# Kernel tuning notes

Measured on AMD Instinct MI355X. Metric: run time of the kernel, lower is better.

## Reference

```python
import jax, jax.numpy as jnp
import numpy as np

# HashGrid config (from ExplicitMaterial.Config defaults)
N_LEVELS = 16
F_PER_LEVEL = 2
TABLE_SIZE = 1 << 19          # log2_hashmap_size = 19
BASE_RES = 16
GROWTH = 1.447269237440378
N_NEURONS = 64                # VanillaMLP hidden width
N_OUT = 3                     # n_output_dims
N_POINTS = 1048576

# 8 trilinear corner offsets, [8,3]
OFFSETS = np.stack(np.meshgrid([0, 1], [0, 1], [0, 1], indexing='ij'), -1).reshape(8, 3)
PRIMES = np.array([1, 2654435761, 805459861], dtype=np.uint32)  # tcnn spatial hash primes


def _level_params():
    # tcnn convention: scale = base * growth^l - 1, resolution = ceil(scale) + 1
    out = []
    for l in range(N_LEVELS):
        scale = BASE_RES * (GROWTH ** l) - 1.0
        res = int(np.ceil(scale)) + 1
        out.append((scale, res))
    return out


def hash_grid_encode(x01, table):
    # x01: [N,3] in [0,1]; table: [L, T, F]
    offsets_u = jnp.asarray(OFFSETS, dtype=jnp.uint32)          # [8,3]
    offsets_f = jnp.asarray(OFFSETS, dtype=x01.dtype)           # [8,3]
    outs = []
    for l, (scale, res) in enumerate(_level_params()):
        pos = x01 * scale + 0.5                                  # [N,3]
        p0f = jnp.floor(pos)
        frac = pos - p0f                                         # [N,3]
        p0 = p0f.astype(jnp.uint32)
        corners = p0[:, None, :] + offsets_u                     # [N,8,3]
        if res ** 3 <= TABLE_SIZE:
            # dense indexing for coarse levels
            c = jnp.minimum(corners, np.uint32(res - 1))
            idx = c[..., 0] + c[..., 1] * np.uint32(res) + c[..., 2] * np.uint32(res * res)
        else:
            # spatial hash: xor of coordinate * prime, masked to table size
            idx = (corners[..., 0] * np.uint32(PRIMES[0])) \
                ^ (corners[..., 1] * np.uint32(PRIMES[1])) \
                ^ (corners[..., 2] * np.uint32(PRIMES[2]))
            idx = idx & np.uint32(TABLE_SIZE - 1)
        feats = table[l][idx]                                    # [N,8,F] gather
        w = jnp.prod(jnp.where(offsets_f[None] > 0, frac[:, None, :], 1.0 - frac[:, None, :]), axis=-1)  # [N,8]
        outs.append(jnp.sum(w[..., None] * feats, axis=1))       # [N,F]
    return jnp.concatenate(outs, axis=-1)                        # [N, L*F]


def setup_inputs() -> dict:
    key = jax.random.key(0)
    k1, k2, k3, k4 = jax.random.split(key, 4)
    positions = jax.random.uniform(k1, (N_POINTS, 3), dtype=jnp.float32, minval=-1.0, maxval=1.0)
    # tcnn init: uniform(-1e-4, 1e-4)
    hash_table = jax.random.uniform(k2, (N_LEVELS, TABLE_SIZE, F_PER_LEVEL), dtype=jnp.float32,
                                    minval=-1e-4, maxval=1e-4)
    d_in = N_LEVELS * F_PER_LEVEL
    w1 = jax.random.normal(k3, (d_in, N_NEURONS), dtype=jnp.float32) * (2.0 / d_in) ** 0.5
    w2 = jax.random.normal(k4, (N_NEURONS, N_OUT), dtype=jnp.float32) * (2.0 / N_NEURONS) ** 0.5
    return {"positions": positions, "hash_table": hash_table, "w1": w1, "w2": w2}


def reference(positions, hash_table, w1, w2):
    # contract_to_unisphere (bounded): scale bbox [-1,1]^3 -> [0,1]^3
    x01 = (positions + 1.0) * 0.5
    enc = hash_grid_encode(x01, hash_table)                      # [N,32]
    h = jax.nn.relu(enc @ w1)                                    # VanillaMLP, bias-free
    feat = h @ w2                                                # output_activation = none
    color = jax.nn.sigmoid(feat)                                 # material_activation
    return color
```

## Files before the change

### kernel.cpp

```cpp
#include <hip/hip_runtime.h>
#include <stdint.h>
#include <math.h>

#define NLEVELS 16
#define NDENSE  5
#define NHASH   11
#define TSIZE   (1u << 19)
#define HMASK   (TSIZE - 1u)
#define PRIME_Y 2654435761u
#define PRIME_Z 805459861u

#define FP8_SCALE 8192.0f
#define FP8_INV   (1.0f / 8192.0f)

typedef float v2f __attribute__((ext_vector_type(2)));

struct Params {
    float    scale[NLEVELS];
    unsigned res[NDENSE];
    unsigned doff[NDENSE];
};

__device__ __forceinline__ unsigned umin_(unsigned a, unsigned b) { return a < b ? a : b; }

__global__ __launch_bounds__(256) void repack_hash8(const float4* __restrict__ src,
                                                    uint2* __restrict__ dst, int n4) {
    const int i = blockIdx.x * 256 + threadIdx.x;
    if (i >= n4) return;
    const float4 a = src[2 * i];
    const float4 b = src[2 * i + 1];
    int lo = __builtin_amdgcn_cvt_pk_fp8_f32(a.x * FP8_SCALE, a.y * FP8_SCALE, 0, false);
    lo     = __builtin_amdgcn_cvt_pk_fp8_f32(a.z * FP8_SCALE, a.w * FP8_SCALE, lo, true);
    int hi = __builtin_amdgcn_cvt_pk_fp8_f32(b.x * FP8_SCALE, b.y * FP8_SCALE, 0, false);
    hi     = __builtin_amdgcn_cvt_pk_fp8_f32(b.z * FP8_SCALE, b.w * FP8_SCALE, hi, true);
    dst[i] = make_uint2((unsigned)lo, (unsigned)hi);
}

__global__ __launch_bounds__(256) void repack_dense8(const float2* __restrict__ table,
                                                     uint2* __restrict__ dst, Params pr) {
    const int l = blockIdx.y;
    const unsigned R = pr.res[l];
    const unsigned n = R * R * R;
    const unsigned e = blockIdx.x * 256 + threadIdx.x;
    if (e >= n) return;
    const unsigned xx = e % R;
    const unsigned t  = e / R;
    const unsigned yy = t % R;
    const unsigned x1 = umin_(xx + 1u, R - 1) - xx;
    const unsigned y1 = (umin_(yy + 1u, R - 1) - yy) * R;
    const float2* src = table + (size_t)l * TSIZE;
    const float2 a = src[e];
    const float2 b = src[e + x1];
    const float2 c = src[e + y1];
    const float2 d = src[e + y1 + x1];
    int w0 = __builtin_amdgcn_cvt_pk_fp8_f32(a.x * FP8_SCALE, a.y * FP8_SCALE, 0, false);
    w0     = __builtin_amdgcn_cvt_pk_fp8_f32(b.x * FP8_SCALE, b.y * FP8_SCALE, w0, true);
    int w1 = __builtin_amdgcn_cvt_pk_fp8_f32(c.x * FP8_SCALE, c.y * FP8_SCALE, 0, false);
    w1     = __builtin_amdgcn_cvt_pk_fp8_f32(d.x * FP8_SCALE, d.y * FP8_SCALE, w1, true);
    dst[pr.doff[l] + e] = make_uint2((unsigned)w0, (unsigned)w1);
}

__device__ __forceinline__ void lvl_tw(float x, float y, float z, float s,
                                       float* wx, float* wy, float* wz) {
    const float fx = fmaf(x, s, 0.5f), fy = fmaf(y, s, 0.5f), fz = fmaf(z, s, 0.5f);
    const float tx = fx - floorf(fx), ty = fy - floorf(fy), tz = fz - floorf(fz);
    wx[0] = 1.f - tx; wx[1] = tx;
    wy[0] = 1.f - ty; wy[1] = ty;
    wz[0] = 1.f - tz; wz[1] = tz;
}

__device__ __forceinline__ void hash_issue_pair(const void* __restrict__ hashTV, int lrel,
                                                float x, float y, float z, float s,
                                                unsigned* __restrict__ U,
                                                unsigned* __restrict__ V,
                                                unsigned* __restrict__ flg) {
    const float fx = fmaf(x, s, 0.5f), fy = fmaf(y, s, 0.5f), fz = fmaf(z, s, 0.5f);
    const unsigned x0 = (unsigned)floorf(fx);
    const unsigned y0 = (unsigned)floorf(fy);
    const unsigned z0 = (unsigned)floorf(fz);
    const unsigned hy0 = y0 * PRIME_Y, hz0 = z0 * PRIME_Z;
    unsigned H[4];
    H[0] = hy0 ^ hz0;
    H[1] = (hy0 + PRIME_Y) ^ hz0;
    H[2] = hy0 ^ (hz0 + PRIME_Z);
    H[3] = (hy0 + PRIME_Y) ^ (hz0 + PRIME_Z);
    *flg = (x0 & 1u) | (((y0 ^ z0) & 1u) << 1);
    if (x0 & 1u) {
        const unsigned short* t8 = (const unsigned short*)hashTV + (size_t)lrel * TSIZE;
#pragma unroll
        for (int c = 0; c < 4; ++c) {
            const unsigned i0 = (x0 ^ H[c]) & HMASK;
            const unsigned i1 = ((x0 + 1u) ^ H[c]) & HMASK;
            U[c] = t8[i0];
            V[c] = t8[i1];
        }
    } else {
        const unsigned* t32 = (const unsigned*)hashTV + (size_t)lrel * (TSIZE / 2);
#pragma unroll
        for (int c = 0; c < 4; ++c) {
            const unsigned i0 = (x0 ^ H[c]) & HMASK;
            U[c] = t32[i0 >> 1];
        }
    }
}

__global__ __launch_bounds__(256) void hgmlp_fp8p(
    const float* __restrict__ gpos,
    const void* __restrict__ hashTV,
    const uint2* __restrict__ denseT,
    const float* __restrict__ gw1,
    const float* __restrict__ gw2,
    float* __restrict__ gout,
    int npts, Params pr)
{
    __shared__ float w1t[64 * 32];
    __shared__ float w2s[64 * 3];
    const int tid = threadIdx.x;
    const int p = blockIdx.x * 256 + tid;

    float px = 0.f, py = 0.f, pz = 0.f;
    if (p < npts) { px = gpos[3 * p]; py = gpos[3 * p + 1]; pz = gpos[3 * p + 2]; }

    for (int e = tid; e < 32 * 64; e += 256) {
        const int i = e & 31, j = e >> 5;
        w1t[e] = gw1[i * 64 + j];
    }
    if (tid < 192) w2s[tid] = gw2[tid];
    __syncthreads();

    if (p >= npts) return;

    const float x = (px + 1.f) * 0.5f;
    const float y = (py + 1.f) * 0.5f;
    const float z = (pz + 1.f) * 0.5f;

    float enc[32];

    uint2 dv[NDENSE][2];
#pragma unroll
    for (int l = 0; l < NDENSE; ++l) {
        const float s = pr.scale[l];
        const unsigned R = pr.res[l];
        const float fx = fmaf(x, s, 0.5f), fy = fmaf(y, s, 0.5f), fz = fmaf(z, s, 0.5f);
        const unsigned x0 = (unsigned)floorf(fx);
        const unsigned y0 = (unsigned)floorf(fy);
        const unsigned z0 = (unsigned)floorf(fz);
        const unsigned base = umin_(x0, R - 1) + umin_(y0, R - 1) * R;
        const unsigned cz0 = umin_(z0, R - 1) * R * R;
        const unsigned cz1 = umin_(z0 + 1u, R - 1) * R * R;
        const uint2* tl = denseT + pr.doff[l];
        dv[l][0] = tl[base + cz0];
        dv[l][1] = tl[base + cz1];
    }

    unsigned U[4][4], V[4][4], flg[4];
    hash_issue_pair(hashTV, 0, x, y, z, pr.scale[5], U[0], V[0], &flg[0]);
    hash_issue_pair(hashTV, 1, x, y, z, pr.scale[6], U[1], V[1], &flg[1]);
    hash_issue_pair(hashTV, 2, x, y, z, pr.scale[7], U[2], V[2], &flg[2]);

#pragma unroll
    for (int l = 0; l < NDENSE; ++l) {
        float wx[2], wy[2], wz[2];
        lvl_tw(x, y, z, pr.scale[l], wx, wy, wz);
        float e0 = 0.f, e1 = 0.f;
#pragma unroll
        for (int dz = 0; dz < 2; ++dz) {
            const uint2 u2 = dv[l][dz];
            const v2f c00 = __builtin_amdgcn_cvt_pk_f32_fp8((int)u2.x, false);
            const v2f c10 = __builtin_amdgcn_cvt_pk_f32_fp8((int)u2.x, true);
            const v2f c01 = __builtin_amdgcn_cvt_pk_f32_fp8((int)u2.y, false);
            const v2f c11 = __builtin_amdgcn_cvt_pk_f32_fp8((int)u2.y, true);
            const float w00 = wz[dz] * wy[0] * wx[0];
            const float w10 = wz[dz] * wy[0] * wx[1];
            const float w01 = wz[dz] * wy[1] * wx[0];
            const float w11 = wz[dz] * wy[1] * wx[1];
            e0 = fmaf(w00, c00.x, fmaf(w10, c10.x, fmaf(w01, c01.x, fmaf(w11, c11.x, e0))));
            e1 = fmaf(w00, c00.y, fmaf(w10, c10.y, fmaf(w01, c01.y, fmaf(w11, c11.y, e1))));
        }
        enc[2 * l + 0] = e0 * FP8_INV;
        enc[2 * l + 1] = e1 * FP8_INV;
    }

#pragma unroll
    for (int l = NDENSE; l < NLEVELS; ++l) {
        if (l + 3 < NLEVELS) {
            const int sl = (l + 3 - NDENSE) & 3;
            hash_issue_pair(hashTV, l + 3 - NDENSE, x, y, z, pr.scale[l + 3],
                            U[sl], V[sl], &flg[sl]);
        }
        const int sl = (l - NDENSE) & 3;
        float wx[2], wy[2], wz[2];
        lvl_tw(x, y, z, pr.scale[l], wx, wy, wz);
        const unsigned xo = flg[sl] & 1u;
        const unsigned pb = (flg[sl] >> 1) & 1u;
        float e0 = 0.f, e1 = 0.f;
#pragma unroll
        for (int c = 0; c < 4; ++c) {
            const unsigned u = U[sl][c];
            const unsigned lo = u & 0xFFFFu, hi = u >> 16;
            const unsigned swp = (xo ^ 1u) & (pb ^ (unsigned)(c & 1) ^ (unsigned)(c >> 1));
            const unsigned ec0 = xo ? lo : (swp ? hi : lo);
            const unsigned ec1 = xo ? (V[sl][c] & 0xFFFFu) : (swp ? lo : hi);
            const v2f f0 = __builtin_amdgcn_cvt_pk_f32_fp8((int)ec0, false);
            const v2f f1 = __builtin_amdgcn_cvt_pk_f32_fp8((int)ec1, false);
            const float wc = wy[c & 1] * wz[c >> 1];
            e0 = fmaf(wc * wx[0], f0.x, fmaf(wc * wx[1], f1.x, e0));
            e1 = fmaf(wc * wx[0], f0.y, fmaf(wc * wx[1], f1.y, e1));
        }
        enc[2 * l + 0] = e0 * FP8_INV;
        enc[2 * l + 1] = e1 * FP8_INV;
    }

    float o0 = 0.f, o1 = 0.f, o2 = 0.f;
    for (int j = 0; j < 64; ++j) {
        const float* wr = &w1t[j * 32];
        float acc = 0.f;
#pragma unroll
        for (int i = 0; i < 32; ++i) acc = fmaf(enc[i], wr[i], acc);
        acc = fmaxf(acc, 0.f);
        o0 = fmaf(acc, w2s[3 * j + 0], o0);
        o1 = fmaf(acc, w2s[3 * j + 1], o1);
        o2 = fmaf(acc, w2s[3 * j + 2], o2);
    }
    gout[3 * p + 0] = 1.f / (1.f + __expf(-o0));
    gout[3 * p + 1] = 1.f / (1.f + __expf(-o1));
    gout[3 * p + 2] = 1.f / (1.f + __expf(-o2));
}

__global__ __launch_bounds__(256) void hgmlp_fp32(
    const float* __restrict__ gpos, const float* __restrict__ gtable,
    const float* __restrict__ gw1, const float* __restrict__ gw2,
    float* __restrict__ gout, int npts, Params pr)
{
    __shared__ float w1t[64 * 32];
    __shared__ float w2s[64 * 3];
    const int tid = threadIdx.x;
    const int p = blockIdx.x * 256 + tid;
    float px = 0.f, py = 0.f, pz = 0.f;
    if (p < npts) { px = gpos[3 * p]; py = gpos[3 * p + 1]; pz = gpos[3 * p + 2]; }
    for (int e = tid; e < 32 * 64; e += 256) { const int i = e & 31, j = e >> 5; w1t[e] = gw1[i * 64 + j]; }
    if (tid < 192) w2s[tid] = gw2[tid];
    __syncthreads();
    if (p >= npts) return;
    const float x = (px + 1.f) * 0.5f, y = (py + 1.f) * 0.5f, z = (pz + 1.f) * 0.5f;
    float enc[32];
#pragma unroll
    for (int l = 0; l < NLEVELS; ++l) {
        const float s = pr.scale[l];
        const float fx = fmaf(x, s, 0.5f), fy = fmaf(y, s, 0.5f), fz = fmaf(z, s, 0.5f);
        const float bx = floorf(fx), by = floorf(fy), bz = floorf(fz);
        const float tx = fx - bx, ty = fy - by, tz = fz - bz;
        const unsigned x0 = (unsigned)bx, y0 = (unsigned)by, z0 = (unsigned)bz;
        const float wx[2] = {1.f - tx, tx}, wy[2] = {1.f - ty, ty}, wz[2] = {1.f - tz, tz};
        const float2* tl = (const float2*)gtable + (size_t)l * TSIZE;
        float e0 = 0.f, e1 = 0.f;
        unsigned idx[8];
        if (l < NDENSE) {
            const unsigned R = pr.res[l];
            const unsigned cx[2] = {umin_(x0, R - 1), umin_(x0 + 1u, R - 1)};
            const unsigned cy[2] = {umin_(y0, R - 1) * R, umin_(y0 + 1u, R - 1) * R};
            const unsigned cz[2] = {umin_(z0, R - 1) * R * R, umin_(z0 + 1u, R - 1) * R * R};
#pragma unroll
            for (int c = 0; c < 8; ++c) idx[c] = cx[c & 1] + cy[(c >> 1) & 1] + cz[c >> 2];
        } else {
            const unsigned hy0 = y0 * PRIME_Y, hz0 = z0 * PRIME_Z;
#pragma unroll
            for (int c = 0; c < 8; ++c)
                idx[c] = ((x0 + (c & 1)) ^ (hy0 + ((c >> 1) & 1) * PRIME_Y) ^ (hz0 + (c >> 2) * PRIME_Z)) & HMASK;
        }
#pragma unroll
        for (int c = 0; c < 8; ++c) {
            const float2 f = tl[idx[c]];
            const float w = wx[c & 1] * wy[(c >> 1) & 1] * wz[c >> 2];
            e0 = fmaf(w, f.x, e0); e1 = fmaf(w, f.y, e1);
        }
        enc[2 * l + 0] = e0; enc[2 * l + 1] = e1;
    }
    float o0 = 0.f, o1 = 0.f, o2 = 0.f;
    for (int j = 0; j < 64; ++j) {
        const float* wr = &w1t[j * 32];
        float acc = 0.f;
#pragma unroll
        for (int i = 0; i < 32; ++i) acc = fmaf(enc[i], wr[i], acc);
        acc = fmaxf(acc, 0.f);
        o0 = fmaf(acc, w2s[3 * j + 0], o0);
        o1 = fmaf(acc, w2s[3 * j + 1], o1);
        o2 = fmaf(acc, w2s[3 * j + 2], o2);
    }
    gout[3 * p + 0] = 1.f / (1.f + __expf(-o0));
    gout[3 * p + 1] = 1.f / (1.f + __expf(-o1));
    gout[3 * p + 2] = 1.f / (1.f + __expf(-o2));
}

extern "C" void kernel_launch(void* const* d_in, const int* in_sizes, int n_in,
                              void* d_out, int out_size, void* d_ws, size_t ws_size,
                              hipStream_t stream)
{
    const float* gpos   = (const float*)d_in[0];
    const float* gtable = (const float*)d_in[1];
    const float* gw1    = (const float*)d_in[2];
    const float* gw2    = (const float*)d_in[3];
    float* gout = (float*)d_out;
    const int npts = in_sizes[0] / 3;

    Params pr;
    unsigned total = 0, maxn = 0;
    for (int l = 0; l < NLEVELS; ++l) {
        const double scale = 16.0 * pow(1.447269237440378, (double)l) - 1.0;
        pr.scale[l] = (float)scale;
        if (l < NDENSE) {
            const unsigned R = (unsigned)ceil(scale) + 1u;
            pr.res[l] = R;
            pr.doff[l] = total;
            total += R * R * R;
            if (R * R * R > maxn) maxn = R * R * R;
        }
    }
    const size_t hash_bytes = (size_t)NHASH * TSIZE * 2u;
    const size_t need = hash_bytes + (size_t)total * 8u;
    const int blocks = (npts + 255) / 256;

    if (ws_size >= need) {
        void* hashTV = d_ws;
        uint2* denseT = (uint2*)((char*)d_ws + hash_bytes);
        const int n4 = NHASH * TSIZE / 4;
        hipLaunchKernelGGL(repack_hash8, dim3((n4 + 255) / 256), dim3(256), 0, stream,
                           (const float4*)((const float2*)gtable + (size_t)NDENSE * TSIZE),
                           (uint2*)hashTV, n4);
        hipLaunchKernelGGL(repack_dense8, dim3((maxn + 255) / 256, NDENSE), dim3(256), 0, stream,
                           (const float2*)gtable, denseT, pr);
        hipLaunchKernelGGL(hgmlp_fp8p, dim3(blocks), dim3(256), 0, stream,
                           gpos, hashTV, denseT, gw1, gw2, gout, npts, pr);
    } else {
        hipLaunchKernelGGL(hgmlp_fp32, dim3(blocks), dim3(256), 0, stream,
                           gpos, gtable, gw1, gw2, gout, npts, pr);
    }
}
```

Measured before the change: 383.3 us.

## Move MLP weights to global, deepen hash prefetch, use packed FMA and staged stores

Transposes the MLP weights once in a separate small kernel and reads them from global memory (scalar/uniform loads) instead of staging them in LDS per block. This removes the per-block weight copy and its barrier. The hash gathers are now issued five levels ahead instead of three, giving more memory-level parallelism at the cost of extra registers. Interpolation and the first MLP layer use packed two-wide FMAs, launch bounds ask for higher occupancy, and outputs go through LDS so full blocks write with coalesced float4 stores. The deeper prefetch and the occupancy hint could cause register spills.

```diff
diff --git a/kernel.cpp b/kernel.cpp
--- a/kernel.cpp
+++ b/kernel.cpp
@@ -22,6 +22,11 @@
 };
 
 __device__ __forceinline__ unsigned umin_(unsigned a, unsigned b) { return a < b ? a : b; }
+
+__device__ __forceinline__ v2f fma2(float w, v2f f, v2f a) {
+    v2f wv = {w, w};
+    return __builtin_elementwise_fma(wv, f, a);
+}
 
 __global__ __launch_bounds__(256) void repack_hash8(const float4* __restrict__ src,
                                                     uint2* __restrict__ dst, int n4) {
@@ -60,6 +65,19 @@
     dst[pr.doff[l] + e] = make_uint2((unsigned)w0, (unsigned)w1);
 }
 
+__global__ __launch_bounds__(256) void repack_w(const float* __restrict__ gw1,
+                                                const float* __restrict__ gw2,
+                                                float* __restrict__ w1t,
+                                                float* __restrict__ w2c) {
+    const int i = blockIdx.x * 256 + threadIdx.x;
+    if (i < 2048) {
+        const int j = i >> 5, k = i & 31;
+        w1t[i] = gw1[k * 64 + j];
+    } else if (i < 2048 + 192) {
+        w2c[i - 2048] = gw2[i - 2048];
+    }
+}
+
 __device__ __forceinline__ void lvl_tw(float x, float y, float z, float s,
                                        float* wx, float* wy, float* wz) {
     const float fx = fmaf(x, s, 0.5f), fy = fmaf(y, s, 0.5f), fz = fmaf(z, s, 0.5f);
@@ -104,37 +122,28 @@
     }
 }
 
-__global__ __launch_bounds__(256) void hgmlp_fp8p(
+__global__ __launch_bounds__(256, 4) void hgmlp_fp8p(
     const float* __restrict__ gpos,
     const void* __restrict__ hashTV,
     const uint2* __restrict__ denseT,
-    const float* __restrict__ gw1,
-    const float* __restrict__ gw2,
+    const float* __restrict__ w1tg,
+    const float* __restrict__ w2g,
     float* __restrict__ gout,
     int npts, Params pr)
 {
-    __shared__ float w1t[64 * 32];
-    __shared__ float w2s[64 * 3];
+    __shared__ __align__(16) float ostage[768];
     const int tid = threadIdx.x;
     const int p = blockIdx.x * 256 + tid;
+    const bool full = (blockIdx.x * 256 + 256) <= npts;
 
     float px = 0.f, py = 0.f, pz = 0.f;
     if (p < npts) { px = gpos[3 * p]; py = gpos[3 * p + 1]; pz = gpos[3 * p + 2]; }
-
-    for (int e = tid; e < 32 * 64; e += 256) {
-        const int i = e & 31, j = e >> 5;
-        w1t[e] = gw1[i * 64 + j];
-    }
-    if (tid < 192) w2s[tid] = gw2[tid];
-    __syncthreads();
-
-    if (p >= npts) return;
 
     const float x = (px + 1.f) * 0.5f;
     const float y = (py + 1.f) * 0.5f;
     const float z = (pz + 1.f) * 0.5f;
 
-    float enc[32];
+    v2f enc[16];
 
     uint2 dv[NDENSE][2];
 #pragma unroll
@@ -153,16 +162,16 @@
         dv[l][1] = tl[base + cz1];
     }
 
-    unsigned U[4][4], V[4][4], flg[4];
-    hash_issue_pair(hashTV, 0, x, y, z, pr.scale[5], U[0], V[0], &flg[0]);
-    hash_issue_pair(hashTV, 1, x, y, z, pr.scale[6], U[1], V[1], &flg[1]);
-    hash_issue_pair(hashTV, 2, x, y, z, pr.scale[7], U[2], V[2], &flg[2]);
+    unsigned U[6][4], V[6][4], flg[6];
+#pragma unroll
+    for (int k = 0; k < 5; ++k)
+        hash_issue_pair(hashTV, k, x, y, z, pr.scale[NDENSE + k], U[k], V[k], &flg[k]);
 
 #pragma unroll
     for (int l = 0; l < NDENSE; ++l) {
         float wx[2], wy[2], wz[2];
         lvl_tw(x, y, z, pr.scale[l], wx, wy, wz);
-        float e0 = 0.f, e1 = 0.f;
+        v2f e = {0.f, 0.f};
 #pragma unroll
         for (int dz = 0; dz < 2; ++dz) {
             const uint2 u2 = dv[l][dz];
@@ -170,30 +179,26 @@
             const v2f c10 = __builtin_amdgcn_cvt_pk_f32_fp8((int)u2.x, true);
             const v2f c01 = __builtin_amdgcn_cvt_pk_f32_fp8((int)u2.y, false);
             const v2f c11 = __builtin_amdgcn_cvt_pk_f32_fp8((int)u2.y, true);
-            const float w00 = wz[dz] * wy[0] * wx[0];
-            const float w10 = wz[dz] * wy[0] * wx[1];
-            const float w01 = wz[dz] * wy[1] * wx[0];
-            const float w11 = wz[dz] * wy[1] * wx[1];
-            e0 = fmaf(w00, c00.x, fmaf(w10, c10.x, fmaf(w01, c01.x, fmaf(w11, c11.x, e0))));
-            e1 = fmaf(w00, c00.y, fmaf(w10, c10.y, fmaf(w01, c01.y, fmaf(w11, c11.y, e1))));
-        }
-        enc[2 * l + 0] = e0 * FP8_INV;
-        enc[2 * l + 1] = e1 * FP8_INV;
+            e = fma2(wz[dz] * wy[0] * wx[0], c00, e);
+            e = fma2(wz[dz] * wy[0] * wx[1], c10, e);
+            e = fma2(wz[dz] * wy[1] * wx[0], c01, e);
+            e = fma2(wz[dz] * wy[1] * wx[1], c11, e);
+        }
+        enc[l] = e * FP8_INV;
     }
 
 #pragma unroll
     for (int l = NDENSE; l < NLEVELS; ++l) {
-        if (l + 3 < NLEVELS) {
-            const int sl = (l + 3 - NDENSE) & 3;
-            hash_issue_pair(hashTV, l + 3 - NDENSE, x, y, z, pr.scale[l + 3],
-                            U[sl], V[sl], &flg[sl]);
-        }
-        const int sl = (l - NDENSE) & 3;
+        if (l < NLEVELS - 5) {
+            hash_issue_pair(hashTV, l, x, y, z, pr.scale[l + 5],
+                            U[l % 6], V[l % 6], &flg[l % 6]);
+        }
+        const int sl = (l - NDENSE) % 6;
         float wx[2], wy[2], wz[2];
         lvl_tw(x, y, z, pr.scale[l], wx, wy, wz);
         const unsigned xo = flg[sl] & 1u;
         const unsigned pb = (flg[sl] >> 1) & 1u;
-        float e0 = 0.f, e1 = 0.f;
+        v2f e = {0.f, 0.f};
 #pragma unroll
         for (int c = 0; c < 4; ++c) {
             const unsigned u = U[sl][c];
@@ -204,27 +209,46 @@
             const v2f f0 = __builtin_amdgcn_cvt_pk_f32_fp8((int)ec0, false);
             const v2f f1 = __builtin_amdgcn_cvt_pk_f32_fp8((int)ec1, false);
             const float wc = wy[c & 1] * wz[c >> 1];
-            e0 = fmaf(wc * wx[0], f0.x, fmaf(wc * wx[1], f1.x, e0));
-            e1 = fmaf(wc * wx[0], f0.y, fmaf(wc * wx[1], f1.y, e1));
-        }
-        enc[2 * l + 0] = e0 * FP8_INV;
-        enc[2 * l + 1] = e1 * FP8_INV;
+            e = fma2(wc * wx[0], f0, e);
+            e = fma2(wc * wx[1], f1, e);
+        }
+        enc[l] = e * FP8_INV;
     }
 
     float o0 = 0.f, o1 = 0.f, o2 = 0.f;
+#pragma unroll 2
     for (int j = 0; j < 64; ++j) {
-        const float* wr = &w1t[j * 32];
-        float acc = 0.f;
-#pragma unroll
-        for (int i = 0; i < 32; ++i) acc = fmaf(enc[i], wr[i], acc);
+        const v2f* wr = (const v2f*)(w1tg + j * 32);
+        v2f a0 = {0.f, 0.f}, a1 = {0.f, 0.f};
+#pragma unroll
+        for (int i = 0; i < 16; i += 2) {
+            a0 = __builtin_elementwise_fma(enc[i],     wr[i],     a0);
+            a1 = __builtin_elementwise_fma(enc[i + 1], wr[i + 1], a1);
+        }
+        float acc = (a0.x + a0.y) + (a1.x + a1.y);
         acc = fmaxf(acc, 0.f);
-        o0 = fmaf(acc, w2s[3 * j + 0], o0);
-        o1 = fmaf(acc, w2s[3 * j + 1], o1);
-        o2 = fmaf(acc, w2s[3 * j + 2], o2);
-    }
-    gout[3 * p + 0] = 1.f / (1.f + __expf(-o0));
-    gout[3 * p + 1] = 1.f / (1.f + __expf(-o1));
-    gout[3 * p + 2] = 1.f / (1.f + __expf(-o2));
+        o0 = fmaf(acc, w2g[3 * j + 0], o0);
+        o1 = fmaf(acc, w2g[3 * j + 1], o1);
+        o2 = fmaf(acc, w2g[3 * j + 2], o2);
+    }
+    const float r0 = 1.f / (1.f + __expf(-o0));
+    const float r1 = 1.f / (1.f + __expf(-o1));
+    const float r2 = 1.f / (1.f + __expf(-o2));
+
+    if (full) {
+        ostage[3 * tid + 0] = r0;
+        ostage[3 * tid + 1] = r1;
+        ostage[3 * tid + 2] = r2;
+        __syncthreads();
+        if (tid < 192) {
+            const float4 v = ((const float4*)ostage)[tid];
+            ((float4*)(gout + (size_t)blockIdx.x * 768))[tid] = v;
+        }
+    } else if (p < npts) {
+        gout[3 * p + 0] = r0;
+        gout[3 * p + 1] = r1;
+        gout[3 * p + 2] = r2;
+    }
 }
 
 __global__ __launch_bounds__(256) void hgmlp_fp32(
@@ -316,21 +340,26 @@
             if (R * R * R > maxn) maxn = R * R * R;
         }
     }
-    const size_t hash_bytes = (size_t)NHASH * TSIZE * 2u;
-    const size_t need = hash_bytes + (size_t)total * 8u;
+    const size_t hash_bytes  = (size_t)NHASH * TSIZE * 2u;
+    const size_t dense_bytes = (size_t)total * 8u;
+    const size_t w_off = (hash_bytes + dense_bytes + 255u) & ~(size_t)255u;
+    const size_t need = w_off + 2048u * 4u + 192u * 4u;
     const int blocks = (npts + 255) / 256;
 
     if (ws_size >= need) {
         void* hashTV = d_ws;
         uint2* denseT = (uint2*)((char*)d_ws + hash_bytes);
+        float* w1tg = (float*)((char*)d_ws + w_off);
+        float* w2g  = w1tg + 2048;
         const int n4 = NHASH * TSIZE / 4;
         hipLaunchKernelGGL(repack_hash8, dim3((n4 + 255) / 256), dim3(256), 0, stream,
                            (const float4*)((const float2*)gtable + (size_t)NDENSE * TSIZE),
                            (uint2*)hashTV, n4);
         hipLaunchKernelGGL(repack_dense8, dim3((maxn + 255) / 256, NDENSE), dim3(256), 0, stream,
                            (const float2*)gtable, denseT, pr);
+        hipLaunchKernelGGL(repack_w, dim3(9), dim3(256), 0, stream, gw1, gw2, w1tg, w2g);
         hipLaunchKernelGGL(hgmlp_fp8p, dim3(blocks), dim3(256), 0, stream,
-                           gpos, hashTV, denseT, gw1, gw2, gout, npts, pr);
+                           gpos, hashTV, denseT, w1tg, w2g, gout, npts, pr);
     } else {
         hipLaunchKernelGGL(hgmlp_fp32, dim3(blocks), dim3(256), 0, stream,
                            gpos, gtable, gw1, gw2, gout, npts, pr);
```

Measured after the change: 463.3 us. 20.9% more time.
